# Kernel tuning notes

Measured on AMD Instinct MI355X. Metric: run time of the kernel, lower is better.

## Reference

```python
import jax, jax.numpy as jnp
import numpy as np

WEIGHT = 1.0
EPS = 1e-10


def _high_mask(h, w):
    # Boolean mask: True = high-frequency region (outside center rectangle after fftshift)
    mask = np.ones((h, w), dtype=np.float32)
    ch, cw = h // 2, w // 2
    mask[ch - h // 8: ch + h // 8, cw - w // 8: cw + w // 8] = 0.0
    return jnp.asarray(mask)


def _high_freq_psd(img):
    # img: (B, 3, H, W) in [-1, 1] -> per-image mean log10 PSD over high-freq region, shape (B,)
    gray = 0.299 * img[:, 0] + 0.587 * img[:, 1] + 0.114 * img[:, 2]  # (B, H, W)
    gray = (gray + 1.0) / 2.0
    fft = jnp.fft.fft2(gray)                       # batched complex FFT over last two dims
    fft = jnp.fft.fftshift(fft, axes=(-2, -1))
    psd_log = jnp.log10(jnp.abs(fft) ** 2 + EPS)   # (B, H, W)
    h, w = gray.shape[-2:]
    mask = _high_mask(h, w)
    return jnp.sum(psd_log * mask, axis=(-2, -1)) / jnp.sum(mask)


def setup_inputs() -> dict:
    key = jax.random.key(0)
    k1, k2 = jax.random.split(key)
    B, C, H, W = 32, 3, 512, 512
    generated = jax.random.normal(k1, (B, C, H, W), dtype=jnp.float32)
    target = jax.random.normal(k2, (B, C, H, W), dtype=jnp.float32)
    return {"generated": generated, "target": target}


def reference(generated, target):
    psd_gen = _high_freq_psd(generated)      # (B,)
    psd_target = _high_freq_psd(target)      # (B,)
    loss = jnp.mean(jnp.abs(psd_gen - psd_target))  # F.l1_loss
    return WEIGHT * loss
```

## Files before the change

kernel.cpp:

```cpp
#include <hip/hip_runtime.h>
#include <hip/hip_bf16.h>
#include <math.h>


__device__ double g_partials[64 * 33 * 4];
__device__ __align__(16) float2 g_wsfall[256 * 512];

__device__ __forceinline__ float2 cadd(float2 a, float2 b){ return make_float2(a.x+b.x, a.y+b.y); }
__device__ __forceinline__ float2 csub(float2 a, float2 b){ return make_float2(a.x-b.x, a.y-b.y); }
__device__ __forceinline__ float2 cmul(float2 a, float2 b){
  return make_float2(fmaf(a.x, b.x, -(a.y*b.y)), fmaf(a.x, b.y, a.y*b.x));
}
__device__ __forceinline__ float2 mul_mi(float2 a){ return make_float2(a.y, -a.x); }

__device__ __forceinline__ void fft8(float2 v[8]){
  const float S = 0.70710678118654752440f;
  float2 c0=cadd(v[0],v[4]), c1=cadd(v[1],v[5]), c2=cadd(v[2],v[6]), c3=cadd(v[3],v[7]);
  float2 d0=csub(v[0],v[4]);
  float2 t1=csub(v[1],v[5]);
  float2 d1=make_float2(S*(t1.x+t1.y), S*(t1.y-t1.x));
  float2 d2=mul_mi(csub(v[2],v[6]));
  float2 t3=csub(v[3],v[7]);
  float2 d3=make_float2(S*(t3.y-t3.x), -S*(t3.x+t3.y));
  float2 e0=cadd(c0,c2), e1=cadd(c1,c3), f0=csub(c0,c2), f1=mul_mi(csub(c1,c3));
  float2 g0=cadd(d0,d2), g1=cadd(d1,d3), h0=csub(d0,d2), h1=mul_mi(csub(d1,d3));
  v[0]=cadd(e0,e1); v[4]=csub(e0,e1);
  v[2]=cadd(f0,f1); v[6]=csub(f0,f1);
  v[1]=cadd(g0,g1); v[5]=csub(g0,g1);
  v[3]=cadd(h0,h1); v[7]=csub(h0,h1);
}

__device__ __forceinline__ void twiddle8(float2 v[8], float ang){
  float sn, cs;
  __sincosf(ang, &sn, &cs);
  float2 w = make_float2(cs, sn);
  float2 wp = w;
  v[1] = cmul(v[1], wp);
  #pragma unroll
  for (int m = 2; m < 8; ++m){ wp = cmul(wp, w); v[m] = cmul(v[m], wp); }
}

__device__ __forceinline__ int padi(int i){ return i + (i >> 3); }

__device__ __forceinline__ void lds_fence(){
  asm volatile("s_waitcnt lgkmcnt(0)" ::: "memory");
  __builtin_amdgcn_sched_barrier(0);
}

__device__ __forceinline__ void fft512(float2 v[8], float* re, float* im, int t){
  const float TW = -6.28318530717958647692f;
  fft8(v);
  twiddle8(v, TW * (float)t * (1.0f/512.0f));
  lds_fence();
  #pragma unroll
  for (int m = 0; m < 8; ++m){ int a = padi(m*64 + t); re[a] = v[m].x; im[a] = v[m].y; }
  lds_fence();
  const int q = t >> 3, n = t & 7;
  #pragma unroll
  for (int j = 0; j < 8; ++j){ int a = padi(q*64 + n + 8*j); v[j].x = re[a]; v[j].y = im[a]; }
  fft8(v);
  twiddle8(v, TW * (float)n * (1.0f/64.0f));
  lds_fence();
  #pragma unroll
  for (int m = 0; m < 8; ++m){ int a = padi(q*64 + m*8 + n); re[a] = v[m].x; im[a] = v[m].y; }
  lds_fence();
  #pragma unroll
  for (int j = 0; j < 8; ++j){ int a = padi(q*64 + n*8 + j); v[j].x = re[a]; v[j].y = im[a]; }
  fft8(v);
}

#define GRAY1(r,g,b) ((fmaf(0.299f,(r), fmaf(0.587f,(g), 0.114f*(b))) + 1.0f)*0.5f)

__global__ __launch_bounds__(256, 3)
void k_rowfft(const float* __restrict__ gen, const float* __restrict__ tgt,
              float2* ws, int img0){
  float2* w = ws ? ws : g_wsfall;
  const int wg   = blockIdx.x;
  const int imgl = wg >> 6;
  const int rg   = wg & 63;
  const int img  = img0 + imgl;
  const int wave = threadIdx.x >> 6, t = threadIdx.x & 63;
  const int pr   = rg*4 + wave;
  const float* src = (img < 32) ? gen : tgt;
  const float* base = src + (size_t)(img & 31) * 786432 + (size_t)pr * 1024;

  __shared__ float stage_all[4][3072];
  float* st = stage_all[wave];

  #pragma unroll
  for (int ch = 0; ch < 3; ++ch){
    const float* pb = base + ch * 262144 + 4*t;
    float* lb = st + ch*1024;
    #pragma unroll
    for (int seg = 0; seg < 4; ++seg){
      __builtin_amdgcn_global_load_lds(
        (const __attribute__((address_space(1))) void*)(pb + seg*256),
        (__attribute__((address_space(3))) void*)(lb + seg*256),
        16, 0, 0);
    }
  }
  asm volatile("s_waitcnt vmcnt(0)" ::: "memory");
  __builtin_amdgcn_sched_barrier(0);

  float2 v[8];
  #pragma unroll
  for (int j = 0; j < 8; ++j){
    const int x = t + 64*j;
    float rA = st[x],        rB = st[512 + x];
    float gA = st[1024 + x], gB = st[1536 + x];
    float bA = st[2048 + x], bB = st[2560 + x];
    v[j] = make_float2(GRAY1(rA, gA, bA), GRAY1(rB, gB, bB));
  }
  fft512(v, st, st + 1024, t);

  float2* dst = w + ((size_t)imgl * 256 + pr) * 512;
  const int off = 8*(t & 7) + (t >> 3);
  #pragma unroll
  for (int j = 0; j < 8; ++j) dst[64*j + off] = v[j];
}

__global__ __launch_bounds__(256)
void k_colfft(const float2* __restrict__ ws, int img0){
  const float2* w = ws ? ws : (const float2*)g_wsfall;
  const int wg   = blockIdx.x;
  const int imgl = wg / 33;
  const int blk  = wg - imgl * 33;
  const int img  = img0 + imgl;
  const int kx0  = blk * 8;
  const int tid  = threadIdx.x;
  const int wave = tid >> 6, t = tid & 63;
  const int ncols = (blk == 32) ? 1 : 8;

  __shared__ float2 own[8][260], mir[8][260];
  __shared__ float re_all[4][576], im_all[4][576];
  float* re = re_all[wave];
  float* im = im_all[wave];

  const float2* zb = w + (size_t)imgl * 131072;
  #pragma unroll
  for (int it = 0; it < 8; ++it){
    const int idx = it*256 + tid;
    const int p = idx >> 3, e = idx & 7;
    own[e][p] = zb[p*512 + kx0 + e];
    mir[e][p] = zb[p*512 + ((512 - (kx0 + e)) & 511)];
  }
  __syncthreads();

  double acc = 0.0;
  for (int ci = 0; ci < 2; ++ci){
    const int e = wave*2 + ci;
    if (e < ncols){
      const int kx = kx0 + e;
      const bool sub_own = (kx <= 63);
      const bool sub_mir = (kx >= 1) & (kx <= 64);
      const float base = (kx == 0 || kx == 256) ? 1.0f : 2.0f;

      float2 v[8];
      const int u = t >> 1;
      const bool odd = (t & 1);
      #pragma unroll
      for (int j = 0; j < 8; ++j){
        const int p = u + 32*j;
        float2 A = own[e][p];
        float2 B = mir[e][p]; B.y = -B.y;
        float2 Fe = make_float2((A.x + B.x)*0.5f, (A.y + B.y)*0.5f);
        float2 Fo = mul_mi(make_float2((A.x - B.x)*0.5f, (A.y - B.y)*0.5f));
        v[j] = odd ? Fo : Fe;
      }
      fft512(v, re, im, t);

      #pragma unroll
      for (int j = 0; j < 8; ++j){
        const bool inS  = (j == 0) | (j == 7);
        const bool inSp = (j == 0) | ((j == 1) & (t == 0)) | ((j == 7) & (t != 0));
        float wgt = base;
        if (sub_own & inS)  wgt -= 1.0f;
        if (sub_mir & inSp) wgt -= 1.0f;
        float m2 = fmaf(v[j].x, v[j].x, fmaf(v[j].y, v[j].y, 1e-10f));
        acc += (double)wgt * (double)log10f(m2);
      }
    }
  }
  #pragma unroll
  for (int off = 32; off; off >>= 1) acc += __shfl_down(acc, off);
  if (t == 0) g_partials[((size_t)img * 33 + blk) * 4 + wave] = acc;
}

__global__ __launch_bounds__(256)
void k_finish(float* __restrict__ out){
  const int tid = threadIdx.x;
  const int img = tid >> 2, part = tid & 3;
  const double* p = g_partials + (size_t)img * 132 + part;
  double s = 0.0;
  for (int k = 0; k < 33; ++k) s += p[4*k];
  __shared__ double sm[256];
  sm[tid] = s;
  __syncthreads();
  if ((tid & 3) == 0){
    double tot = sm[tid] + sm[tid+1] + sm[tid+2] + sm[tid+3];
    sm[tid] = tot * (1.0 / 245760.0);
  }
  __syncthreads();
  if (tid < 64){
    double dv = (tid < 32) ? fabs(sm[tid*4] - sm[(tid+32)*4]) : 0.0;
    #pragma unroll
    for (int off = 32; off; off >>= 1) dv += __shfl_down(dv, off);
    if (tid == 0) out[0] = (float)(dv * (1.0 / 32.0));
  }
}

extern "C" void kernel_launch(void* const* d_in, const int* in_sizes, int n_in,
                              void* d_out, int out_size, void* d_ws, size_t ws_size,
                              hipStream_t stream){
  (void)in_sizes; (void)n_in; (void)out_size;
  const float* gen = (const float*)d_in[0];
  const float* tgt = (const float*)d_in[1];
  float* out = (float*)d_out;

  const size_t per_img = (size_t)256 * 512 * sizeof(float2);
  int chunk = (int)(ws_size / per_img);
  float2* wsp = (float2*)d_ws;
  if (chunk < 1){ chunk = 1; wsp = nullptr; }
  if (chunk > 64) chunk = 64;

  for (int i0 = 0; i0 < 64; i0 += chunk){
    const int n = (64 - i0 < chunk) ? (64 - i0) : chunk;
    k_rowfft<<<dim3(n * 64), dim3(256), 0, stream>>>(gen, tgt, wsp, i0);
    k_colfft<<<dim3(n * 33), dim3(256), 0, stream>>>(wsp, i0);
  }
  k_finish<<<dim3(1), dim3(256), 0, stream>>>(out);
}
```

Measured before the change: 74.79 us.

## Store intermediate row-FFT spectrum as fp16 and double-buffer row loads per wave

The intermediate workspace between the row FFT and the column FFT now holds half2 values instead of float2, halving its write and read traffic. The row kernel is restructured so each 64-thread wave handles eight row pairs in sequence. While one pair is being transformed, the next pair is prefetched into a second LDS buffer using explicit vmcnt waits. The fp16 storage loses precision in the spectrum, and the log-PSD of large low-frequency values could overflow or lose accuracy. The smaller grid (fewer, longer-lived blocks) may also change occupancy.

```diff
diff --git a/kernel.cpp b/kernel.cpp
--- a/kernel.cpp
+++ b/kernel.cpp
@@ -1,10 +1,11 @@
 #include <hip/hip_runtime.h>
 #include <hip/hip_bf16.h>
+#include <hip/hip_fp16.h>
 #include <math.h>
 
 
 __device__ double g_partials[64 * 33 * 4];
-__device__ __align__(16) float2 g_wsfall[256 * 512];
+__device__ __align__(16) __half2 g_wsfall[256 * 512];
 
 __device__ __forceinline__ float2 cadd(float2 a, float2 b){ return make_float2(a.x+b.x, a.y+b.y); }
 __device__ __forceinline__ float2 csub(float2 a, float2 b){ return make_float2(a.x-b.x, a.y-b.y); }
@@ -71,22 +72,7 @@
 
 #define GRAY1(r,g,b) ((fmaf(0.299f,(r), fmaf(0.587f,(g), 0.114f*(b))) + 1.0f)*0.5f)
 
-__global__ __launch_bounds__(256, 3)
-void k_rowfft(const float* __restrict__ gen, const float* __restrict__ tgt,
-              float2* ws, int img0){
-  float2* w = ws ? ws : g_wsfall;
-  const int wg   = blockIdx.x;
-  const int imgl = wg >> 6;
-  const int rg   = wg & 63;
-  const int img  = img0 + imgl;
-  const int wave = threadIdx.x >> 6, t = threadIdx.x & 63;
-  const int pr   = rg*4 + wave;
-  const float* src = (img < 32) ? gen : tgt;
-  const float* base = src + (size_t)(img & 31) * 786432 + (size_t)pr * 1024;
-
-  __shared__ float stage_all[4][3072];
-  float* st = stage_all[wave];
-
+__device__ __forceinline__ void dma_pair(const float* base, float* st, int t){
   #pragma unroll
   for (int ch = 0; ch < 3; ++ch){
     const float* pb = base + ch * 262144 + 4*t;
@@ -99,29 +85,57 @@
         16, 0, 0);
     }
   }
-  asm volatile("s_waitcnt vmcnt(0)" ::: "memory");
-  __builtin_amdgcn_sched_barrier(0);
-
-  float2 v[8];
-  #pragma unroll
-  for (int j = 0; j < 8; ++j){
-    const int x = t + 64*j;
-    float rA = st[x],        rB = st[512 + x];
-    float gA = st[1024 + x], gB = st[1536 + x];
-    float bA = st[2048 + x], bB = st[2560 + x];
-    v[j] = make_float2(GRAY1(rA, gA, bA), GRAY1(rB, gB, bB));
-  }
-  fft512(v, st, st + 1024, t);
-
-  float2* dst = w + ((size_t)imgl * 256 + pr) * 512;
+}
+
+__global__ __launch_bounds__(128)
+void k_rowfft(const float* __restrict__ gen, const float* __restrict__ tgt,
+              __half2* ws, int img0){
+  __half2* w = ws ? ws : g_wsfall;
+  const int wg   = blockIdx.x;
+  const int imgl = wg >> 4;
+  const int bl   = wg & 15;
+  const int img  = img0 + imgl;
+  const int wave = threadIdx.x >> 6, t = threadIdx.x & 63;
+  const int prB  = bl*16 + wave*8;
+  const float* src = (img < 32) ? gen : tgt;
+  const float* base0 = src + (size_t)(img & 31) * 786432 + (size_t)prB * 1024;
+
+  __shared__ float stage_all[2][2][3072];
+  float* stg0 = stage_all[wave][0];
+  float* stg1 = stage_all[wave][1];
+
   const int off = 8*(t & 7) + (t >> 3);
-  #pragma unroll
-  for (int j = 0; j < 8; ++j) dst[64*j + off] = v[j];
+
+  dma_pair(base0, stg0, t);
+  #pragma unroll
+  for (int n = 0; n < 8; ++n){
+    float* stc = (n & 1) ? stg1 : stg0;
+    float* stn = (n & 1) ? stg0 : stg1;
+    lds_fence();
+    if (n < 7) dma_pair(base0 + (size_t)(n+1)*1024, stn, t);
+    if (n == 0)      { asm volatile("s_waitcnt vmcnt(12)" ::: "memory"); }
+    else if (n < 7)  { asm volatile("s_waitcnt vmcnt(20)" ::: "memory"); }
+    else             { asm volatile("s_waitcnt vmcnt(8)"  ::: "memory"); }
+    __builtin_amdgcn_sched_barrier(0);
+
+    float2 v[8];
+    #pragma unroll
+    for (int j = 0; j < 8; ++j){
+      const int x = t + 64*j;
+      v[j] = make_float2(GRAY1(stc[x],     stc[1024+x], stc[2048+x]),
+                         GRAY1(stc[512+x], stc[1536+x], stc[2560+x]));
+    }
+    fft512(v, stc, stc + 1024, t);
+
+    __half2* dst = w + ((size_t)imgl * 256 + (prB + n)) * 512;
+    #pragma unroll
+    for (int j = 0; j < 8; ++j) dst[64*j + off] = __floats2half2_rn(v[j].x, v[j].y);
+  }
 }
 
 __global__ __launch_bounds__(256)
-void k_colfft(const float2* __restrict__ ws, int img0){
-  const float2* w = ws ? ws : (const float2*)g_wsfall;
+void k_colfft(const __half2* __restrict__ ws, int img0){
+  const __half2* w = ws ? ws : (const __half2*)g_wsfall;
   const int wg   = blockIdx.x;
   const int imgl = wg / 33;
   const int blk  = wg - imgl * 33;
@@ -136,13 +150,13 @@
   float* re = re_all[wave];
   float* im = im_all[wave];
 
-  const float2* zb = w + (size_t)imgl * 131072;
+  const __half2* zb = w + (size_t)imgl * 131072;
   #pragma unroll
   for (int it = 0; it < 8; ++it){
     const int idx = it*256 + tid;
     const int p = idx >> 3, e = idx & 7;
-    own[e][p] = zb[p*512 + kx0 + e];
-    mir[e][p] = zb[p*512 + ((512 - (kx0 + e)) & 511)];
+    own[e][p] = __half22float2(zb[p*512 + kx0 + e]);
+    mir[e][p] = __half22float2(zb[p*512 + ((512 - (kx0 + e)) & 511)]);
   }
   __syncthreads();
 
@@ -217,15 +231,15 @@
   const float* tgt = (const float*)d_in[1];
   float* out = (float*)d_out;
 
-  const size_t per_img = (size_t)256 * 512 * sizeof(float2);
+  const size_t per_img = (size_t)256 * 512 * sizeof(__half2);
   int chunk = (int)(ws_size / per_img);
-  float2* wsp = (float2*)d_ws;
+  __half2* wsp = (__half2*)d_ws;
   if (chunk < 1){ chunk = 1; wsp = nullptr; }
   if (chunk > 64) chunk = 64;
 
   for (int i0 = 0; i0 < 64; i0 += chunk){
     const int n = (64 - i0 < chunk) ? (64 - i0) : chunk;
-    k_rowfft<<<dim3(n * 64), dim3(256), 0, stream>>>(gen, tgt, wsp, i0);
+    k_rowfft<<<dim3(n * 16), dim3(128), 0, stream>>>(gen, tgt, wsp, i0);
     k_colfft<<<dim3(n * 33), dim3(256), 0, stream>>>(wsp, i0);
   }
   k_finish<<<dim3(1), dim3(256), 0, stream>>>(out);
```

After: 72.44 us. 3.2% less time.
